# Performance work log

Measured on AMD Instinct MI355X. Metric: run time of the kernel, lower is better.

Reference implementation:

```python
import jax, jax.numpy as jnp
import numpy as np

B, N, D = 16, 1024, 768
MU = 768
R = 16
DR = D // R  # 48


def _dyn_linear(x, mu, Wg, bg, Bg, bb, in_f, out_f):
    """DynamicLinear: per-sample weights generated from mu via a hypernetwork.
    Wg: [MU, out_f*in_f], bg: [out_f*in_f], Bg: [MU, out_f], bb: [out_f].
    x: [B, in_f] or [B, N, in_f].
    """
    Bsz = mu.shape[0]
    W = (mu @ Wg + bg).reshape(Bsz, out_f, in_f)  # [B, out, in]
    b = mu @ Bg + bb                              # [B, out]
    if x.ndim == 2:
        return jnp.einsum('bi,boi->bo', x, W) + b
    return jnp.einsum('bni,boi->bno', x, W) + b[:, None, :]


def setup_inputs() -> dict:
    key = jax.random.key(0)
    ks = jax.random.split(key, 12)
    s = 0.02
    return {
        'x': jax.random.normal(ks[0], (B, N, D), jnp.float32),
        'mu': jax.random.normal(ks[1], (B, MU), jnp.float32),
        # ChannelGate MLP layer 1: D -> D//R
        'Wg1': jax.random.normal(ks[2], (MU, DR * D), jnp.float32) * s,
        'bg1': jnp.zeros((DR * D,), jnp.float32),
        'Bg1': jax.random.normal(ks[3], (MU, DR), jnp.float32) * s,
        'bb1': jnp.zeros((DR,), jnp.float32),
        # ChannelGate MLP layer 2: D//R -> D
        'Wg2': jax.random.normal(ks[4], (MU, D * DR), jnp.float32) * s,
        'bg2': jnp.zeros((D * DR,), jnp.float32),
        'Bg2': jax.random.normal(ks[5], (MU, D), jnp.float32) * s,
        'bb2': jnp.zeros((D,), jnp.float32),
        # SpatialGate: D -> 1
        'Wgs': jax.random.normal(ks[6], (MU, D), jnp.float32) * s,
        'bgs': jnp.zeros((D,), jnp.float32),
        'Bgs': jax.random.normal(ks[7], (MU, 1), jnp.float32) * s,
        'bbs': jnp.zeros((1,), jnp.float32),
    }


def reference(x, mu, Wg1, bg1, Bg1, bb1, Wg2, bg2, Bg2, bb2, Wgs, bgs, Bgs, bbs):
    def mlp(p):  # p: [B, D]
        h = jax.nn.relu(_dyn_linear(p, mu, Wg1, bg1, Bg1, bb1, D, DR))
        return _dyn_linear(h, mu, Wg2, bg2, Bg2, bb2, DR, D)

    # ChannelGate: avg + max pooling over token dim, shared dynamic MLP
    avg_pool = jnp.mean(x, axis=1)          # [B, D]
    max_pool = jnp.max(x, axis=1)           # [B, D]
    channel_att = mlp(avg_pool) + mlp(max_pool)
    x = x * jax.nn.sigmoid(channel_att)[:, None, :]

    # SpatialGate: per-token dynamic scalar gate
    s = _dyn_linear(x, mu, Wgs, bgs, Bgs, bbs, D, 1)  # [B, N, 1]
    return x * jax.nn.sigmoid(s)
```

## Files before the change

kernel.cpp:

```cpp
#include <hip/hip_runtime.h>
#include <math.h>


#define B_  16
#define N_  1024
#define D_  768
#define MU_ 768

__device__ __forceinline__ void dma16(const float* g, float* l) {
    __builtin_amdgcn_global_load_lds(
        (__attribute__((address_space(1))) void*)(g),
        (__attribute__((address_space(3))) void*)(l), 16, 0, 0);
}

__global__ __launch_bounds__(192) void k_pool(
    const float* __restrict__ x, const float* __restrict__ mu,
    float* __restrict__ mu_t, float* __restrict__ psum, float* __restrict__ pmax)
{
    int blk = blockIdx.x;
    if (blk == 512) {
        for (int e = threadIdx.x; e < MU_ * B_; e += 192) {
            int m = e >> 4, b = e & 15;
            mu_t[e] = mu[b * MU_ + m];
        }
        return;
    }
    int b = blk >> 5, c = blk & 31;
    int d4 = threadIdx.x << 2;
    const float* xp = x + ((size_t)(b * N_ + c * 32)) * D_ + d4;
    float s0 = 0.f, s1 = 0.f, s2 = 0.f, s3 = 0.f;
    float m0 = -3.4e38f, m1 = -3.4e38f, m2 = -3.4e38f, m3 = -3.4e38f;
    for (int n = 0; n < 32; ++n) {
        float4 v = *(const float4*)(xp + (size_t)n * D_);
        s0 += v.x; s1 += v.y; s2 += v.z; s3 += v.w;
        m0 = fmaxf(m0, v.x); m1 = fmaxf(m1, v.y);
        m2 = fmaxf(m2, v.z); m3 = fmaxf(m3, v.w);
    }
    size_t o = ((size_t)(c * B_ + b)) * D_ + d4;
    float4 sv = { s0, s1, s2, s3 }; *(float4*)(psum + o) = sv;
    float4 mv = { m0, m1, m2, m3 }; *(float4*)(pmax + o) = mv;
}

__global__ __launch_bounds__(256, 4) void k_hyper(
    const float* __restrict__ Wg1, const float* __restrict__ bg1,
    const float* __restrict__ Wg2, const float* __restrict__ bg2,
    const float* __restrict__ Wgs, const float* __restrict__ bgs,
    const float* __restrict__ Bg2, const float* __restrict__ bb2,
    const float* __restrict__ mu_t,
    float* __restrict__ w1o, float* __restrict__ w2o,
    float* __restrict__ wso, float* __restrict__ b2o)
{
    __shared__ __align__(16) float ldsW[2][32 * 128];
    __shared__ __align__(16) float ldsMu[2][32 * 16];
    int t = blockIdx.x, tid = threadIdx.x;
    int w = tid >> 6, ln = tid & 63;

    const float* mat; const float* bias; float* outp; int ncols; int tile;
    if (t < 288)      { mat = Wg1; bias = bg1; outp = w1o; ncols = 36864; tile = t; }
    else if (t < 576) { mat = Wg2; bias = bg2; outp = w2o; ncols = 36864; tile = t - 288; }
    else if (t < 582) { mat = Wgs; bias = bgs; outp = wso; ncols = 768;   tile = t - 576; }
    else              { mat = Bg2; bias = bb2; outp = b2o; ncols = 768;   tile = t - 582; }
    int colbase = tile << 7;

    const float* srcW = mat + (size_t)((w << 3) + (ln >> 5)) * ncols
                            + colbase + ((ln & 31) << 2);
    const float* srcMu = mu_t + (ln << 2);
    float* dstW0 = &ldsW[0][w << 10];
    float* dstW1 = &ldsW[1][w << 10];

    #define STAGE(BUF, TT) { \
        const float* s_ = srcW + (size_t)((TT) * 32) * ncols; \
        float* d_ = (BUF) ? dstW1 : dstW0; \
        dma16(s_,                       d_);       \
        dma16(s_ + (size_t)2 * ncols,   d_ + 256); \
        dma16(s_ + (size_t)4 * ncols,   d_ + 512); \
        dma16(s_ + (size_t)6 * ncols,   d_ + 768); \
        if (w == 0) { \
            const float* sm_ = srcMu + (TT) * 512; \
            dma16(sm_,       &ldsMu[BUF][0]);   \
            dma16(sm_ + 256, &ldsMu[BUF][256]); \
        } \
    }

    int c  = tid & 127;
    int bh = tid >> 7;
    float acc[8];
    #pragma unroll
    for (int i = 0; i < 8; ++i) acc[i] = 0.f;

    STAGE(0, 0)
    asm volatile("s_waitcnt vmcnt(0)" ::: "memory");
    __syncthreads();

    for (int tt = 0; tt < 24; ++tt) {
        int cur = tt & 1;
        if (tt < 23) STAGE(cur ^ 1, tt + 1)
        const float* Wb  = &ldsW[cur][0];
        const float* Mb  = &ldsMu[cur][bh << 3];
        #pragma unroll
        for (int m = 0; m < 32; ++m) {
            float wv = Wb[m * 128 + c];
            float4 mA = *(const float4*)(Mb + m * 16);
            float4 mB = *(const float4*)(Mb + m * 16 + 4);
            acc[0] = fmaf(mA.x, wv, acc[0]);
            acc[1] = fmaf(mA.y, wv, acc[1]);
            acc[2] = fmaf(mA.z, wv, acc[2]);
            acc[3] = fmaf(mA.w, wv, acc[3]);
            acc[4] = fmaf(mB.x, wv, acc[4]);
            acc[5] = fmaf(mB.y, wv, acc[5]);
            acc[6] = fmaf(mB.z, wv, acc[6]);
            acc[7] = fmaf(mB.w, wv, acc[7]);
        }
        asm volatile("s_waitcnt vmcnt(0)" ::: "memory");
        __syncthreads();
    }
    #undef STAGE

    float bv = bias[colbase + c];
    #pragma unroll
    for (int i = 0; i < 8; ++i)
        outp[(size_t)((bh << 3) + i) * ncols + colbase + c] = acc[i] + bv;
}

__global__ __launch_bounds__(128) void k_red(
    const float* __restrict__ psum, const float* __restrict__ pmax,
    const float* __restrict__ mu, const float* __restrict__ Bgs,
    const float* __restrict__ bbs,
    float* __restrict__ avgb, float* __restrict__ maxb, float* __restrict__ bs)
{
    int b = blockIdx.x / 6, tile = blockIdx.x % 6, tid = threadIdx.x;
    int d = tile * 128 + tid;
    float s = 0.f, mx = -3.4e38f;
    for (int c = 0; c < 32; ++c) {
        size_t idx = ((size_t)(c * B_ + b)) * D_ + d;
        s += psum[idx];
        mx = fmaxf(mx, pmax[idx]);
    }
    avgb[b * D_ + d] = s * (1.f / 1024.f);
    maxb[b * D_ + d] = mx;

    if (tile == 0) {
        __shared__ float sb[128];
        float p = 0.f;
        for (int m = tid; m < MU_; m += 128) p += mu[b * MU_ + m] * Bgs[m];
        sb[tid] = p;
        __syncthreads();
        if (tid < 64) {
            float v = sb[tid] + sb[tid + 64];
            #pragma unroll
            for (int k = 32; k; k >>= 1) v += __shfl_xor(v, k, 64);
            if (tid == 0) bs[b] = v + bbs[0];
        }
    }
}

__global__ __launch_bounds__(64) void k_c1(
    const float* __restrict__ w1, const float* __restrict__ avgb,
    const float* __restrict__ maxb, const float* __restrict__ mu,
    const float* __restrict__ Bg1, const float* __restrict__ bb1,
    float* __restrict__ g)
{
    int b = blockIdx.x / 48, o = blockIdx.x % 48, ln = threadIdx.x;
    const float* row = w1 + (size_t)b * 36864 + o * 768;
    const float* av  = avgb + b * D_;
    const float* mxp = maxb + b * D_;
    const float* mub = mu + b * MU_;
    float pa = 0.f, pm = 0.f, pb = 0.f;
    #pragma unroll
    for (int i = 0; i < 12; ++i) {
        int idx = ln + (i << 6);
        float wv = row[idx];
        pa += wv * av[idx];
        pm += wv * mxp[idx];
        pb += Bg1[(size_t)idx * 48 + o] * mub[idx];
    }
    #pragma unroll
    for (int k = 32; k; k >>= 1) {
        pa += __shfl_xor(pa, k, 64);
        pm += __shfl_xor(pm, k, 64);
        pb += __shfl_xor(pb, k, 64);
    }
    if (ln == 0) {
        float bb = pb + bb1[o];
        g[b * 48 + o] = fmaxf(pa + bb, 0.f) + fmaxf(pm + bb, 0.f);
    }
}

__global__ __launch_bounds__(64) void k_c2(
    const float* __restrict__ w2, const float* __restrict__ b2w,
    const float* __restrict__ g, float* __restrict__ cg)
{
    __shared__ float gL[48];
    int b = blockIdx.x / 12, tile = blockIdx.x % 12, ln = threadIdx.x;
    if (ln < 48) gL[ln] = g[b * 48 + ln];
    __syncthreads();
    int d = (tile << 6) + ln;
    const float* row = w2 + (size_t)b * 36864 + d * 48;
    float att = 0.f;
    #pragma unroll
    for (int o = 0; o < 48; o += 4) {
        float4 w4 = *(const float4*)(row + o);
        att += w4.x * gL[o] + w4.y * gL[o + 1] + w4.z * gL[o + 2] + w4.w * gL[o + 3];
    }
    att += 2.f * b2w[b * D_ + d];
    cg[b * D_ + d] = 1.f / (1.f + expf(-att));
}

__global__ __launch_bounds__(256) void k_final(
    const float* __restrict__ x, const float* __restrict__ cg,
    const float* __restrict__ wsw, const float* __restrict__ bs,
    float* __restrict__ out)
{
    int wv = threadIdx.x >> 6, ln = threadIdx.x & 63;
    int tok = (blockIdx.x << 2) + wv;
    int b = tok >> 10;
    const float* xp = x + (size_t)tok * D_;
    const float* cp = cg + b * D_;
    const float* wp = wsw + b * D_;
    float xg[12];
    float part = 0.f;
    #pragma unroll
    for (int q = 0; q < 3; ++q) {
        int d = (q << 8) + (ln << 2);
        float4 xv = *(const float4*)(xp + d);
        float4 cv = *(const float4*)(cp + d);
        float4 w4 = *(const float4*)(wp + d);
        float g0 = xv.x * cv.x, g1 = xv.y * cv.y;
        float g2 = xv.z * cv.z, g3 = xv.w * cv.w;
        part += g0 * w4.x + g1 * w4.y + g2 * w4.z + g3 * w4.w;
        xg[q * 4 + 0] = g0; xg[q * 4 + 1] = g1;
        xg[q * 4 + 2] = g2; xg[q * 4 + 3] = g3;
    }
    #pragma unroll
    for (int k = 32; k; k >>= 1) part += __shfl_xor(part, k, 64);
    float s = part + bs[b];
    float sig = 1.f / (1.f + expf(-s));
    #pragma unroll
    for (int q = 0; q < 3; ++q) {
        int d = (q << 8) + (ln << 2);
        float4 o4 = { xg[q * 4 + 0] * sig, xg[q * 4 + 1] * sig,
                      xg[q * 4 + 2] * sig, xg[q * 4 + 3] * sig };
        *(float4*)(out + (size_t)tok * D_ + d) = o4;
    }
}

extern "C" void kernel_launch(void* const* d_in, const int* in_sizes, int n_in,
                              void* d_out, int out_size, void* d_ws, size_t ws_size,
                              hipStream_t stream)
{
    const float* x   = (const float*)d_in[0];
    const float* mu  = (const float*)d_in[1];
    const float* Wg1 = (const float*)d_in[2];
    const float* bg1 = (const float*)d_in[3];
    const float* Bg1 = (const float*)d_in[4];
    const float* bb1 = (const float*)d_in[5];
    const float* Wg2 = (const float*)d_in[6];
    const float* bg2 = (const float*)d_in[7];
    const float* Bg2 = (const float*)d_in[8];
    const float* bb2 = (const float*)d_in[9];
    const float* Wgs = (const float*)d_in[10];
    const float* bgs = (const float*)d_in[11];
    const float* Bgs = (const float*)d_in[12];
    const float* bbs = (const float*)d_in[13];
    float* base = (float*)d_ws;
    float* out  = (float*)d_out;

    float* mu_t = base;
    float* psum = mu_t + 12288;
    float* pmax = psum + 393216;
    float* w1   = pmax + 393216;
    float* w2   = w1   + 589824;
    float* wsw  = w2   + 589824;
    float* b2   = wsw  + 12288;
    float* avgb = b2   + 12288;
    float* maxb = avgb + 12288;
    float* g    = maxb + 12288;
    float* bs   = g    + 768;
    float* cg   = bs   + 16;

    hipLaunchKernelGGL(k_pool,  dim3(513),  dim3(192), 0, stream, x, mu, mu_t, psum, pmax);
    hipLaunchKernelGGL(k_hyper, dim3(588),  dim3(256), 0, stream,
                       Wg1, bg1, Wg2, bg2, Wgs, bgs, Bg2, bb2,
                       mu_t, w1, w2, wsw, b2);
    hipLaunchKernelGGL(k_red,   dim3(96),   dim3(128), 0, stream,
                       psum, pmax, mu, Bgs, bbs, avgb, maxb, bs);
    hipLaunchKernelGGL(k_c1,    dim3(768),  dim3(64),  0, stream,
                       w1, avgb, maxb, mu, Bg1, bb1, g);
    hipLaunchKernelGGL(k_c2,    dim3(192),  dim3(64),  0, stream, w2, b2, g, cg);
    hipLaunchKernelGGL(k_final, dim3(4096), dim3(256), 0, stream, x, cg, wsw, bs, out);
}
```

Before: 112.0 us.

## Retile hypernetwork GEMM to 4x4 register blocks with wave-uniform mu loads

Result: slower. 135.9 us (+21.3%).

```diff
diff --git a/kernel.cpp b/kernel.cpp
--- a/kernel.cpp
+++ b/kernel.cpp
@@ -41,7 +41,7 @@
     float4 mv = { m0, m1, m2, m3 }; *(float4*)(pmax + o) = mv;
 }
 
-__global__ __launch_bounds__(256, 4) void k_hyper(
+__global__ __launch_bounds__(256) void k_hyper(
     const float* __restrict__ Wg1, const float* __restrict__ bg1,
     const float* __restrict__ Wg2, const float* __restrict__ bg2,
     const float* __restrict__ Wgs, const float* __restrict__ bgs,
@@ -50,76 +50,77 @@
     float* __restrict__ w1o, float* __restrict__ w2o,
     float* __restrict__ wso, float* __restrict__ b2o)
 {
-    __shared__ __align__(16) float ldsW[2][32 * 128];
-    __shared__ __align__(16) float ldsMu[2][32 * 16];
+    __shared__ __align__(16) float ldsW[2][16 * 256];
     int t = blockIdx.x, tid = threadIdx.x;
     int w = tid >> 6, ln = tid & 63;
 
-    const float* mat; const float* bias; float* outp; int ncols; int tile;
-    if (t < 288)      { mat = Wg1; bias = bg1; outp = w1o; ncols = 36864; tile = t; }
-    else if (t < 576) { mat = Wg2; bias = bg2; outp = w2o; ncols = 36864; tile = t - 288; }
-    else if (t < 582) { mat = Wgs; bias = bgs; outp = wso; ncols = 768;   tile = t - 576; }
-    else              { mat = Bg2; bias = bb2; outp = b2o; ncols = 768;   tile = t - 582; }
-    int colbase = tile << 7;
-
-    const float* srcW = mat + (size_t)((w << 3) + (ln >> 5)) * ncols
-                            + colbase + ((ln & 31) << 2);
-    const float* srcMu = mu_t + (ln << 2);
-    float* dstW0 = &ldsW[0][w << 10];
-    float* dstW1 = &ldsW[1][w << 10];
+    const float* mat; const float* bias; float* outp; int ncols; int colbase;
+    if (t < 144)      { mat = Wg1; bias = bg1; outp = w1o; ncols = 36864; colbase = t << 8; }
+    else if (t < 288) { mat = Wg2; bias = bg2; outp = w2o; ncols = 36864; colbase = (t - 144) << 8; }
+    else if (t < 291) { mat = Wgs; bias = bgs; outp = wso; ncols = 768;   colbase = (t - 288) << 8; }
+    else              { mat = Bg2; bias = bb2; outp = b2o; ncols = 768;   colbase = (t - 291) << 8; }
+
+    const float* srcW = mat + colbase + (ln << 2) + (size_t)(w << 2) * ncols;
 
     #define STAGE(BUF, TT) { \
-        const float* s_ = srcW + (size_t)((TT) * 32) * ncols; \
-        float* d_ = (BUF) ? dstW1 : dstW0; \
-        dma16(s_,                       d_);       \
-        dma16(s_ + (size_t)2 * ncols,   d_ + 256); \
-        dma16(s_ + (size_t)4 * ncols,   d_ + 512); \
-        dma16(s_ + (size_t)6 * ncols,   d_ + 768); \
-        if (w == 0) { \
-            const float* sm_ = srcMu + (TT) * 512; \
-            dma16(sm_,       &ldsMu[BUF][0]);   \
-            dma16(sm_ + 256, &ldsMu[BUF][256]); \
-        } \
-    }
-
-    int c  = tid & 127;
-    int bh = tid >> 7;
-    float acc[8];
-    #pragma unroll
-    for (int i = 0; i < 8; ++i) acc[i] = 0.f;
+        const float* s_ = srcW + (size_t)((TT) << 4) * ncols; \
+        float* d_ = &ldsW[BUF][w << 10]; \
+        dma16(s_,                     d_);       \
+        dma16(s_ + ncols,             d_ + 256); \
+        dma16(s_ + (size_t)2 * ncols, d_ + 512); \
+        dma16(s_ + (size_t)3 * ncols, d_ + 768); \
+    }
+
+    int ct = tid & 63;
+    int bqu = __builtin_amdgcn_readfirstlane(tid >> 6);
+    const float* mus = mu_t + (bqu << 2);
+
+    float4 acc[4];
+    #pragma unroll
+    for (int i = 0; i < 4; ++i) acc[i] = make_float4(0.f, 0.f, 0.f, 0.f);
 
     STAGE(0, 0)
     asm volatile("s_waitcnt vmcnt(0)" ::: "memory");
     __syncthreads();
 
-    for (int tt = 0; tt < 24; ++tt) {
+    for (int tt = 0; tt < 48; ++tt) {
         int cur = tt & 1;
-        if (tt < 23) STAGE(cur ^ 1, tt + 1)
-        const float* Wb  = &ldsW[cur][0];
-        const float* Mb  = &ldsMu[cur][bh << 3];
+        if (tt < 47) STAGE(cur ^ 1, tt + 1)
+        const float* Wb = &ldsW[cur][ct << 2];
+        const float* mrow = mus + ((tt << 4) << 4);
         #pragma unroll
-        for (int m = 0; m < 32; ++m) {
-            float wv = Wb[m * 128 + c];
-            float4 mA = *(const float4*)(Mb + m * 16);
-            float4 mB = *(const float4*)(Mb + m * 16 + 4);
-            acc[0] = fmaf(mA.x, wv, acc[0]);
-            acc[1] = fmaf(mA.y, wv, acc[1]);
-            acc[2] = fmaf(mA.z, wv, acc[2]);
-            acc[3] = fmaf(mA.w, wv, acc[3]);
-            acc[4] = fmaf(mB.x, wv, acc[4]);
-            acc[5] = fmaf(mB.y, wv, acc[5]);
-            acc[6] = fmaf(mB.z, wv, acc[6]);
-            acc[7] = fmaf(mB.w, wv, acc[7]);
+        for (int k = 0; k < 16; ++k) {
+            float4 wv = *(const float4*)(Wb + (k << 8));
+            float4 mv = *(const float4*)(mrow + (k << 4));
+            acc[0].x = fmaf(mv.x, wv.x, acc[0].x);
+            acc[0].y = fmaf(mv.x, wv.y, acc[0].y);
+            acc[0].z = fmaf(mv.x, wv.z, acc[0].z);
+            acc[0].w = fmaf(mv.x, wv.w, acc[0].w);
+            acc[1].x = fmaf(mv.y, wv.x, acc[1].x);
+            acc[1].y = fmaf(mv.y, wv.y, acc[1].y);
+            acc[1].z = fmaf(mv.y, wv.z, acc[1].z);
+            acc[1].w = fmaf(mv.y, wv.w, acc[1].w);
+            acc[2].x = fmaf(mv.z, wv.x, acc[2].x);
+            acc[2].y = fmaf(mv.z, wv.y, acc[2].y);
+            acc[2].z = fmaf(mv.z, wv.z, acc[2].z);
+            acc[2].w = fmaf(mv.z, wv.w, acc[2].w);
+            acc[3].x = fmaf(mv.w, wv.x, acc[3].x);
+            acc[3].y = fmaf(mv.w, wv.y, acc[3].y);
+            acc[3].z = fmaf(mv.w, wv.z, acc[3].z);
+            acc[3].w = fmaf(mv.w, wv.w, acc[3].w);
         }
         asm volatile("s_waitcnt vmcnt(0)" ::: "memory");
         __syncthreads();
     }
     #undef STAGE
 
-    float bv = bias[colbase + c];
-    #pragma unroll
-    for (int i = 0; i < 8; ++i)
-        outp[(size_t)((bh << 3) + i) * ncols + colbase + c] = acc[i] + bv;
+    float4 bv = *(const float4*)(bias + colbase + (ct << 2));
+    #pragma unroll
+    for (int i = 0; i < 4; ++i) {
+        float4 o = acc[i];
+        o.x += bv.x; o.y += bv.y; o.z += bv.z; o.w += bv.w;
+        *(float4*)(outp + (size_t)((bqu << 2) + i) * ncols + colbase + (ct << 2)) = o;
+    }
 }
 
 __global__ __launch_bounds__(128) void k_red(
@@ -279,7 +280,7 @@
     float* cg   = bs   + 16;
 
     hipLaunchKernelGGL(k_pool,  dim3(513),  dim3(192), 0, stream, x, mu, mu_t, psum, pmax);
-    hipLaunchKernelGGL(k_hyper, dim3(588),  dim3(256), 0, stream,
+    hipLaunchKernelGGL(k_hyper, dim3(294),  dim3(256), 0, stream,
                        Wg1, bg1, Wg2, bg2, Wgs, bgs, Bg2, bb2,
                        mu_t, w1, w2, wsw, b2);
     hipLaunchKernelGGL(k_red,   dim3(96),   dim3(128), 0, stream,
```
